# Kernel optimization log

Measured on AMD Instinct MI355X. Metric: run time of the kernel, lower is better.

The kernel has to match this reference:

```python
import jax, jax.numpy as jnp
import numpy as np

B = 32768
K = 8           # moe_num_experts
LATENT = 256    # latent_dim
COND = 1024     # fusion_hidden_dim
HID = 128       # moe_expert_hidden_dim
EIN = LATENT + COND + 1  # expert input dim = 1281


def setup_inputs() -> dict:
    key = jax.random.key(0)
    ks = jax.random.split(key, 12)
    cond = jax.random.normal(ks[0], (B, COND), dtype=jnp.float32)
    u = jax.random.normal(ks[1], (B, LATENT), dtype=jnp.float32)
    tau = jax.random.uniform(ks[2], (B, 1), dtype=jnp.float32)
    # posterior gate: positive, sums to 1 over K (realistic p_hat)
    p_raw = jax.random.uniform(ks[3], (B, K), dtype=jnp.float32)
    p_hat = p_raw / jnp.sum(p_raw, axis=-1, keepdims=True)
    s = 0.02
    W1 = jax.random.normal(ks[4], (K, EIN, HID), dtype=jnp.float32) * s
    b1 = jnp.zeros((K, HID), dtype=jnp.float32)
    W2 = jax.random.normal(ks[5], (K, HID, HID), dtype=jnp.float32) * s
    b2 = jnp.zeros((K, HID), dtype=jnp.float32)
    W3 = jax.random.normal(ks[6], (K, HID, LATENT), dtype=jnp.float32) * s
    b3 = jnp.zeros((K, LATENT), dtype=jnp.float32)
    return {"cond": cond, "u": u, "tau": tau, "p_hat": p_hat,
            "W1": W1, "b1": b1, "W2": W2, "b2": b2, "W3": W3, "b3": b3}


def reference(cond, u, tau, p_hat, W1, b1, W2, b2, W3, b3):
    # Training path: gate = p_hat (no smooth switching, no running gate).
    x = jnp.concatenate([u, cond, tau], axis=-1)           # (B, EIN)
    h = jax.nn.silu(jnp.einsum('bd,kdh->bkh', x, W1) + b1) # (B, K, HID)
    h = jax.nn.silu(jnp.einsum('bkh,khg->bkg', h, W2) + b2)
    v_experts = jnp.einsum('bkg,kgl->bkl', h, W3) + b3     # (B, K, LATENT)
    v = jnp.einsum('bk,bkl->bl', p_hat, v_experts)         # (B, LATENT)
    return v
```

## Files before the change

### kernel.cpp

```cpp
#include <hip/hip_runtime.h>
#include <stdint.h>

typedef unsigned short u16;
typedef __attribute__((ext_vector_type(8))) short short8;
typedef __attribute__((ext_vector_type(4))) float f32x4;
typedef __attribute__((ext_vector_type(4))) uint32_t u32x4;

#define KEXP   8
#define LATENT 256
#define CONDD  1024
#define HID    128
#define EIN    1281
#define EINP   1344
#define NCH    21
#define NTOT   1024
#define BROWS  32768

__device__ __forceinline__ u16 f2bf(float x) {
  uint32_t v = __float_as_uint(x);
  v += 0x7fffu + ((v >> 16) & 1u);
  return (u16)(v >> 16);
}

__device__ __forceinline__ void async16(const void* g, void* l) {
  __builtin_amdgcn_global_load_lds(
      (const __attribute__((address_space(1))) void*)g,
      (__attribute__((address_space(3))) void*)l, 16, 0, 0);
}

__device__ __forceinline__ float silu(float x) { return x / (1.f + __expf(-x)); }

#define W1_TILES (KEXP * 42 * 4)
#define W2_TILES (KEXP * 4 * 4)
#define W3_TILES (KEXP * 4 * 8)
#define WCONV_TILES (W1_TILES + W2_TILES + W3_TILES)
#define XGRP (BROWS * 168)
#define XBLK (XGRP / 256)

__global__ __launch_bounds__(256)
void prep(const float* __restrict__ W1, const float* __restrict__ W2,
          const float* __restrict__ W3, const float* __restrict__ cond,
          const float* __restrict__ uu, const float* __restrict__ tau,
          u16* __restrict__ W1t, u16* __restrict__ W2t, u16* __restrict__ W3t2,
          u16* __restrict__ Xbf) {
  __shared__ float t[32][33];
  const int bid = blockIdx.x;
  if (bid >= WCONV_TILES) {
    int g = (bid - WCONV_TILES) * 256 + threadIdx.x;
    int row = g / 168;
    int c8  = g - row * 168;
    float f0 = 0.f, f1 = 0.f, f2 = 0.f, f3 = 0.f, f4 = 0.f, f5 = 0.f, f6 = 0.f, f7 = 0.f;
    if (c8 < 32) {
      const float4* p = (const float4*)(uu + (size_t)row * LATENT + c8 * 8);
      float4 a = p[0], b = p[1];
      f0 = a.x; f1 = a.y; f2 = a.z; f3 = a.w; f4 = b.x; f5 = b.y; f6 = b.z; f7 = b.w;
    } else if (c8 < 160) {
      const float4* p = (const float4*)(cond + (size_t)row * CONDD + (c8 - 32) * 8);
      float4 a = p[0], b = p[1];
      f0 = a.x; f1 = a.y; f2 = a.z; f3 = a.w; f4 = b.x; f5 = b.y; f6 = b.z; f7 = b.w;
    } else if (c8 == 160) {
      f0 = tau[row];
    }
    u32x4 pk;
    pk[0] = (uint32_t)f2bf(f0) | ((uint32_t)f2bf(f1) << 16);
    pk[1] = (uint32_t)f2bf(f2) | ((uint32_t)f2bf(f3) << 16);
    pk[2] = (uint32_t)f2bf(f4) | ((uint32_t)f2bf(f5) << 16);
    pk[3] = (uint32_t)f2bf(f6) | ((uint32_t)f2bf(f7) << 16);
    *(u32x4*)(Xbf + (size_t)row * EINP + c8 * 8) = pk;
    return;
  }
  const int tx = threadIdx.x & 31, ty = threadIdx.x >> 5;
  if (bid < W1_TILES) {
    int k = bid / 168, r = bid % 168;
    int d0 = (r / 4) * 32, h0 = (r % 4) * 32;
    const float* src = W1 + (size_t)k * EIN * HID;
    #pragma unroll
    for (int s = 0; s < 4; ++s) {
      int d = d0 + ty + s * 8;
      t[ty + s * 8][tx] = (d < EIN) ? src[(size_t)d * HID + h0 + tx] : 0.f;
    }
    __syncthreads();
    u16* dst = W1t + (size_t)k * HID * EINP;
    #pragma unroll
    for (int s = 0; s < 4; ++s)
      dst[(size_t)(h0 + ty + s * 8) * EINP + d0 + tx] = f2bf(t[tx][ty + s * 8]);
  } else if (bid < W1_TILES + W2_TILES) {
    int j = bid - W1_TILES;
    int k = j / 16, r = j % 16;
    int d0 = (r / 4) * 32, h0 = (r % 4) * 32;
    const float* src = W2 + (size_t)k * HID * HID;
    #pragma unroll
    for (int s = 0; s < 4; ++s)
      t[ty + s * 8][tx] = src[(size_t)(d0 + ty + s * 8) * HID + h0 + tx];
    __syncthreads();
    u16* dst = W2t + (size_t)k * HID * HID;
    #pragma unroll
    for (int s = 0; s < 4; ++s)
      dst[(size_t)(h0 + ty + s * 8) * HID + d0 + tx] = f2bf(t[tx][ty + s * 8]);
  } else {
    int j = bid - W1_TILES - W2_TILES;
    int k = j / 32, r = j % 32;
    int d0 = (r / 8) * 32, h0 = (r % 8) * 32;
    const float* src = W3 + (size_t)k * HID * LATENT;
    #pragma unroll
    for (int s = 0; s < 4; ++s)
      t[ty + s * 8][tx] = src[(size_t)(d0 + ty + s * 8) * LATENT + h0 + tx];
    __syncthreads();
    #pragma unroll
    for (int s = 0; s < 4; ++s)
      W3t2[(size_t)(h0 + ty + s * 8) * NTOT + k * HID + d0 + tx] = f2bf(t[tx][ty + s * 8]);
  }
}

__global__ __launch_bounds__(256, 2)
void h1_fused(const u16* __restrict__ Xbf, const u16* __restrict__ W1t,
              const float* __restrict__ b1, const u16* __restrict__ W2t,
              const float* __restrict__ b2, const float* __restrict__ p_hat,
              u16* __restrict__ H) {
  __shared__ union {
    struct { u16 As[3][8192]; u16 Bs[2][8192]; } s;
    struct { u16 As2[16384]; u16 Bs2[2][8192]; } g;
    u16 Cs[128 * 72];
  } sm;

  const int tid  = threadIdx.x;
  const int wave = tid >> 6;
  const int lane = tid & 63;
  const int q    = lane >> 4;
  const int ln   = lane & 15;
  const int wm   = wave >> 1, wn = wave & 1;
  const int bid  = blockIdx.x;
  const int mt   = ((bid >> 6) << 3) | (bid & 7);
  const int e    = (bid >> 3) & 7;
  const int m0   = mt * 128;
  const u16* w1k = W1t + (size_t)e * HID * EINP;
  const u16* xtb = Xbf + (size_t)m0 * EINP;

  const f32x4 fz = {0.f, 0.f, 0.f, 0.f};
  f32x4 acc[4][4];
  #pragma unroll
  for (int m = 0; m < 4; ++m)
    #pragma unroll
    for (int n = 0; n < 4; ++n) acc[m][n] = fz;

  const int rloc = lane >> 3;
  const int gsw  = lane & 7;
  const int gsrc = gsw ^ rloc;

#define H1_SA(d0, buf) { \
  _Pragma("unroll") \
  for (int i_ = 0; i_ < 4; ++i_) { \
    int rb_ = (wave * 4 + i_) * 8; \
    async16(xtb + (size_t)(rb_ + rloc) * EINP + (d0) + gsrc * 8, &sm.s.As[buf][rb_ * 64]); \
  } }
#define H1_SB(d0, buf) { \
  _Pragma("unroll") \
  for (int i_ = 0; i_ < 4; ++i_) { \
    int rb_ = (wave * 4 + i_) * 8; \
    async16(w1k + (size_t)(rb_ + rloc) * EINP + (d0) + gsrc * 8, &sm.s.Bs[buf][rb_ * 64]); \
  } }

  auto mfma_chunk = [&](const u16* Ab, const u16* Bb) {
    __builtin_amdgcn_s_setprio(1);
    #pragma unroll
    for (int ks = 0; ks < 2; ++ks) {
      short8 a[4], b[4];
      #pragma unroll
      for (int m = 0; m < 4; ++m) {
        int r = wm * 64 + m * 16 + ln;
        int g = (ks * 4 + q) ^ (r & 7);
        a[m] = *(const short8*)(&Ab[r * 64 + g * 8]);
      }
      #pragma unroll
      for (int n = 0; n < 4; ++n) {
        int c = wn * 64 + n * 16 + ln;
        int g = (ks * 4 + q) ^ (c & 7);
        b[n] = *(const short8*)(&Bb[c * 64 + g * 8]);
      }
      #pragma unroll
      for (int m = 0; m < 4; ++m)
        #pragma unroll
        for (int n = 0; n < 4; ++n)
          acc[m][n] = __builtin_amdgcn_mfma_f32_16x16x32_bf16(a[m], b[n], acc[m][n], 0, 0, 0);
    }
    __builtin_amdgcn_s_setprio(0);
  };

#define H1_CH(trel, ac, bc, bp, ap, vm) \
  H1_SB(db + ((trel) + 1) * 64, bp); \
  H1_SA(db + ((trel) + 2) * 64, ap); \
  mfma_chunk(sm.s.As[ac], sm.s.Bs[bc]); \
  asm volatile("s_waitcnt vmcnt(" #vm ")" ::: "memory"); \
  __builtin_amdgcn_s_barrier(); \
  __builtin_amdgcn_sched_barrier(0);

  H1_SA(0, 0); H1_SB(0, 0); H1_SA(64, 1);
  asm volatile("s_waitcnt vmcnt(4)" ::: "memory");
  __builtin_amdgcn_s_barrier();
  __builtin_amdgcn_sched_barrier(0);

  #pragma unroll 1
  for (int j = 0; j < 3; ++j) {
    const int db = j * 384;
    H1_CH(0, 0, 0, 1, 2, 4)
    H1_CH(1, 1, 1, 0, 0, 4)
    H1_CH(2, 2, 0, 1, 1, 4)
    H1_CH(3, 0, 1, 0, 2, 4)
    H1_CH(4, 1, 0, 1, 0, 4)
    H1_CH(5, 2, 1, 0, 1, 4)
  }
  {
    const int db = 1152;
    H1_CH(0, 0, 0, 1, 2, 4)
    H1_SB(db + 128, 0);
    mfma_chunk(sm.s.As[1], sm.s.Bs[1]);
    asm volatile("s_waitcnt vmcnt(0)" ::: "memory");
    __builtin_amdgcn_s_barrier();
    __builtin_amdgcn_sched_barrier(0);
    mfma_chunk(sm.s.As[2], sm.s.Bs[0]);
  }
  __syncthreads();

  const u16* w2k = W2t + (size_t)e * HID * HID;
  #pragma unroll
  for (int kc = 0; kc < 2; ++kc)
    #pragma unroll
    for (int i = 0; i < 4; ++i) {
      int rbase = (wave * 4 + i) * 8;
      async16(w2k + (size_t)(rbase + rloc) * HID + kc * 64 + gsrc * 8,
              &sm.g.Bs2[kc][rbase * 64]);
    }

  float pr[4][4];
  #pragma unroll
  for (int m = 0; m < 4; ++m)
    #pragma unroll
    for (int r = 0; r < 4; ++r)
      pr[m][r] = p_hat[(size_t)(m0 + wm * 64 + m * 16 + q * 4 + r) * KEXP + e];

  #pragma unroll
  for (int n = 0; n < 4; ++n) {
    int cl = wn * 64 + n * 16 + ln;
    float bv = b1[e * HID + cl];
    #pragma unroll
    for (int m = 0; m < 4; ++m)
      #pragma unroll
      for (int r = 0; r < 4; ++r) {
        int row = wm * 64 + m * 16 + q * 4 + r;
        sm.g.As2[row * 128 + (((cl >> 3) ^ (row & 7)) << 3) + (cl & 7)] =
            f2bf(silu(acc[m][n][r] + bv));
      }
  }

  f32x4 acc2[4][4];
  #pragma unroll
  for (int m = 0; m < 4; ++m)
    #pragma unroll
    for (int n = 0; n < 4; ++n) acc2[m][n] = fz;

  __syncthreads();

  #pragma unroll
  for (int kc = 0; kc < 2; ++kc) {
    #pragma unroll
    for (int ks = 0; ks < 2; ++ks) {
      short8 a[4], b[4];
      #pragma unroll
      for (int m = 0; m < 4; ++m) {
        int r = wm * 64 + m * 16 + ln;
        int G = kc * 8 + ks * 4 + q;
        int g = (G & 8) | ((G ^ (r & 7)) & 7);
        a[m] = *(const short8*)(&sm.g.As2[r * 128 + g * 8]);
      }
      #pragma unroll
      for (int n = 0; n < 4; ++n) {
        int c = wn * 64 + n * 16 + ln;
        int g = (ks * 4 + q) ^ (c & 7);
        b[n] = *(const short8*)(&sm.g.Bs2[kc][c * 64 + g * 8]);
      }
      #pragma unroll
      for (int m = 0; m < 4; ++m)
        #pragma unroll
        for (int n = 0; n < 4; ++n)
          acc2[m][n] = __builtin_amdgcn_mfma_f32_16x16x32_bf16(a[m], b[n], acc2[m][n], 0, 0, 0);
    }
  }
  __syncthreads();

  u16* hb = H + (size_t)m0 * NTOT + e * HID;
  #pragma unroll 1
  for (int hf = 0; hf < 2; ++hf) {
    if (wn == hf) {
      #pragma unroll
      for (int n = 0; n < 4; ++n) {
        int cl = n * 16 + ln;
        float bv = b2[e * HID + hf * 64 + cl];
        #pragma unroll
        for (int m = 0; m < 4; ++m)
          #pragma unroll
          for (int r = 0; r < 4; ++r) {
            int row = wm * 64 + m * 16 + q * 4 + r;
            sm.Cs[row * 72 + cl] = f2bf(pr[m][r] * silu(acc2[m][n][r] + bv));
          }
      }
    }
    __syncthreads();
    #pragma unroll
    for (int i = 0; i < 4; ++i) {
      int lin = tid + i * 256;
      int row = lin >> 3;
      int grp = lin & 7;
      *(u32x4*)(hb + (size_t)row * NTOT + hf * 64 + grp * 8) =
          *(const u32x4*)(&sm.Cs[row * 72 + grp * 8]);
    }
    __syncthreads();
  }
#undef H1_SA
#undef H1_SB
#undef H1_CH
}

__global__ __launch_bounds__(256, 2)
void out_gemm(const u16* __restrict__ H, const float* __restrict__ p_hat,
              const u16* __restrict__ W3t2, const float* __restrict__ b3,
              float* __restrict__ out) {
  __shared__ struct {
    u16 As[3][4096];
    u16 Bs[3][8192];
    float Ps[64 * 8];
    float B3s[128 * 8];
  } sm;

  const int tid  = threadIdx.x;
  const int wave = tid >> 6;
  const int lane = tid & 63;
  const int q    = lane >> 4;
  const int ln   = lane & 15;
  const int bid  = blockIdx.x;
  const int mt   = ((bid >> 4) << 3) | (bid & 7);
  const int bn   = (bid >> 3) & 1;
  const int m0   = mt * 64, n0 = bn * 128;

  if (tid < 128) {
    int row = tid >> 1, h = tid & 1;
    *(float4*)(&sm.Ps[row * 8 + h * 4]) = *(const float4*)(p_hat + (size_t)(m0 + row) * KEXP + h * 4);
  }
  #pragma unroll
  for (int i = 0; i < 4; ++i) {
    int k = i * 2 + (tid >> 7);
    int c = tid & 127;
    sm.B3s[c * 8 + k] = b3[k * LATENT + n0 + c];
  }

  const f32x4 fz = {0.f, 0.f, 0.f, 0.f};
  f32x4 acc[4][2];
  #pragma unroll
  for (int m = 0; m < 4; ++m) { acc[m][0] = fz; acc[m][1] = fz; }

  const int rloc = lane >> 3;
  const int gsw  = lane & 7;
  const int gsrc = gsw ^ rloc;

#define OG_SA(d0, buf) { \
  _Pragma("unroll") \
  for (int i_ = 0; i_ < 2; ++i_) { \
    int rb_ = (wave * 2 + i_) * 8; \
    async16(H + (size_t)(m0 + rb_ + rloc) * NTOT + (d0) + gsrc * 8, &sm.As[buf][rb_ * 64]); \
  } }
#define OG_SB(d0, buf) { \
  _Pragma("unroll") \
  for (int i_ = 0; i_ < 4; ++i_) { \
    int rb_ = (wave * 4 + i_) * 8; \
    async16(W3t2 + (size_t)(n0 + rb_ + rloc) * NTOT + (d0) + gsrc * 8, &sm.Bs[buf][rb_ * 64]); \
  } }

  auto mfma_chunk = [&](const u16* Ab, const u16* Bb) {
    __builtin_amdgcn_s_setprio(1);
    #pragma unroll
    for (int ks = 0; ks < 2; ++ks) {
      short8 a[4], b[2];
      #pragma unroll
      for (int m = 0; m < 4; ++m) {
        int r = m * 16 + ln;
        int g = (ks * 4 + q) ^ (r & 7);
        a[m] = *(const short8*)(&Ab[r * 64 + g * 8]);
      }
      #pragma unroll
      for (int n = 0; n < 2; ++n) {
        int c = wave * 32 + n * 16 + ln;
        int g = (ks * 4 + q) ^ (c & 7);
        b[n] = *(const short8*)(&Bb[c * 64 + g * 8]);
      }
      #pragma unroll
      for (int m = 0; m < 4; ++m)
        #pragma unroll
        for (int n = 0; n < 2; ++n)
          acc[m][n] = __builtin_amdgcn_mfma_f32_16x16x32_bf16(a[m], b[n], acc[m][n], 0, 0, 0);
    }
    __builtin_amdgcn_s_setprio(0);
  };

#define OG_CH(trel, ac, ap) \
  OG_SB(db + ((trel) + 2) * 64, ap); \
  OG_SA(db + ((trel) + 2) * 64, ap); \
  mfma_chunk(sm.As[ac], sm.Bs[ac]); \
  asm volatile("s_waitcnt vmcnt(6)" ::: "memory"); \
  __builtin_amdgcn_s_barrier(); \
  __builtin_amdgcn_sched_barrier(0);

  OG_SA(0, 0); OG_SB(0, 0);
  OG_SA(64, 1); OG_SB(64, 1);
  asm volatile("s_waitcnt vmcnt(6)" ::: "memory");
  __builtin_amdgcn_s_barrier();
  __builtin_amdgcn_sched_barrier(0);

  #pragma unroll 1
  for (int j = 0; j < 4; ++j) {
    const int db = j * 192;
    OG_CH(0, 0, 2)
    OG_CH(1, 1, 0)
    OG_CH(2, 2, 1)
  }
  {
    const int db = 768;
    OG_CH(0, 0, 2)
    OG_CH(1, 1, 0)
    mfma_chunk(sm.As[2], sm.Bs[2]);
    asm volatile("s_waitcnt vmcnt(0)" ::: "memory");
    __builtin_amdgcn_s_barrier();
    __builtin_amdgcn_sched_barrier(0);
    mfma_chunk(sm.As[0], sm.Bs[0]);
  }

  #pragma unroll
  for (int n = 0; n < 2; ++n) {
    int col = wave * 32 + n * 16 + ln;
    float4 c0 = *(const float4*)(&sm.B3s[col * 8]);
    float4 c1 = *(const float4*)(&sm.B3s[col * 8 + 4]);
    #pragma unroll
    for (int m = 0; m < 4; ++m)
      #pragma unroll
      for (int r = 0; r < 4; ++r) {
        int row = m * 16 + q * 4 + r;
        float4 p0 = *(const float4*)(&sm.Ps[row * 8]);
        float4 p1 = *(const float4*)(&sm.Ps[row * 8 + 4]);
        float v = acc[m][n][r]
                + p0.x * c0.x + p0.y * c0.y + p0.z * c0.z + p0.w * c0.w
                + p1.x * c1.x + p1.y * c1.y + p1.z * c1.z + p1.w * c1.w;
        out[(size_t)(m0 + row) * LATENT + n0 + col] = v;
      }
  }
#undef OG_SA
#undef OG_SB
#undef OG_CH
}

__global__ __launch_bounds__(256, 4)
void h1_gemm(const float* __restrict__ cond, const float* __restrict__ uu,
             const float* __restrict__ tau, const u16* __restrict__ W1t,
             const float* __restrict__ b1, u16* __restrict__ H1) {
  __shared__ union {
    struct { u16 As[128 * 64]; u16 Bs[128 * 64]; } s;
    u16 Cs[128 * 72];
  } sm;

  const int tid  = threadIdx.x;
  const int wave = tid >> 6;
  const int lane = tid & 63;
  const int q    = lane >> 4;
  const int ln   = lane & 15;
  const int wm   = wave >> 1, wn = wave & 1;
  const int bid  = blockIdx.x;
  const int mt   = ((bid >> 6) << 3) | (bid & 7);
  const int e    = (bid >> 3) & 7;
  const int m0   = mt * 128, n0 = e * 128;
  const u16* w1k = W1t + (size_t)e * HID * EINP;

  const f32x4 fz = {0.f, 0.f, 0.f, 0.f};
  f32x4 acc[4][4];
  #pragma unroll
  for (int m = 0; m < 4; ++m)
    #pragma unroll
    for (int n = 0; n < 4; ++n) acc[m][n] = fz;

  #pragma unroll 1
  for (int ic = 0; ic < NCH; ++ic) {
    const int d0 = ic * 64;
    #pragma unroll
    for (int i = 0; i < 4; ++i) {
      int lin  = tid + i * 256;
      int row  = lin >> 3;
      int gsw  = lin & 7;
      int gsrc = gsw ^ (row & 7);
      int gr   = m0 + row;
      float f0, f1, f2, f3, f4, f5, f6, f7;
      if (d0 < 256) {
        const float4* p = (const float4*)(uu + (size_t)gr * LATENT + d0 + gsrc * 8);
        float4 A = p[0], Bv = p[1];
        f0 = A.x; f1 = A.y; f2 = A.z; f3 = A.w; f4 = Bv.x; f5 = Bv.y; f6 = Bv.z; f7 = Bv.w;
      } else if (d0 < 1280) {
        const float4* p = (const float4*)(cond + (size_t)gr * CONDD + (d0 - 256) + gsrc * 8);
        float4 A = p[0], Bv = p[1];
        f0 = A.x; f1 = A.y; f2 = A.z; f3 = A.w; f4 = Bv.x; f5 = Bv.y; f6 = Bv.z; f7 = Bv.w;
      } else {
        float tv = tau[gr];
        f0 = (gsrc == 0) ? tv : 0.f;
        f1 = f2 = f3 = f4 = f5 = f6 = f7 = 0.f;
      }
      u32x4 pk;
      pk[0] = (uint32_t)f2bf(f0) | ((uint32_t)f2bf(f1) << 16);
      pk[1] = (uint32_t)f2bf(f2) | ((uint32_t)f2bf(f3) << 16);
      pk[2] = (uint32_t)f2bf(f4) | ((uint32_t)f2bf(f5) << 16);
      pk[3] = (uint32_t)f2bf(f6) | ((uint32_t)f2bf(f7) << 16);
      *(u32x4*)(&sm.s.As[row * 64 + gsw * 8]) = pk;
    }
    {
      int rloc = lane >> 3;
      int gsw  = lane & 7;
      int gsrc = gsw ^ rloc;
      #pragma unroll
      for (int i = 0; i < 4; ++i) {
        int rbase = (wave * 4 + i) * 8;
        async16(w1k + (size_t)(rbase + rloc) * EINP + d0 + gsrc * 8,
                &sm.s.Bs[rbase * 64]);
      }
    }
    __syncthreads();
    #pragma unroll
    for (int ks = 0; ks < 2; ++ks) {
      short8 a[4], b[4];
      #pragma unroll
      for (int m = 0; m < 4; ++m) {
        int r = wm * 64 + m * 16 + ln;
        int g = (ks * 4 + q) ^ (r & 7);
        a[m] = *(const short8*)(&sm.s.As[r * 64 + g * 8]);
      }
      #pragma unroll
      for (int n = 0; n < 4; ++n) {
        int c = wn * 64 + n * 16 + ln;
        int g = (ks * 4 + q) ^ (c & 7);
        b[n] = *(const short8*)(&sm.s.Bs[c * 64 + g * 8]);
      }
      #pragma unroll
      for (int m = 0; m < 4; ++m)
        #pragma unroll
        for (int n = 0; n < 4; ++n)
          acc[m][n] = __builtin_amdgcn_mfma_f32_16x16x32_bf16(a[m], b[n], acc[m][n], 0, 0, 0);
    }
    __syncthreads();
  }

  #pragma unroll 1
  for (int hf = 0; hf < 2; ++hf) {
    if (wn == hf) {
      #pragma unroll
      for (int n = 0; n < 4; ++n) {
        int cl = n * 16 + ln;
        float bv = b1[n0 + hf * 64 + cl];
        #pragma unroll
        for (int m = 0; m < 4; ++m)
          #pragma unroll
          for (int r = 0; r < 4; ++r)
            sm.Cs[(wm * 64 + m * 16 + q * 4 + r) * 72 + cl] = f2bf(silu(acc[m][n][r] + bv));
      }
    }
    __syncthreads();
    #pragma unroll
    for (int i = 0; i < 4; ++i) {
      int lin = tid + i * 256;
      int row = lin >> 3;
      int grp = lin & 7;
      *(u32x4*)(H1 + (size_t)(m0 + row) * NTOT + n0 + hf * 64 + grp * 8) =
          *(const u32x4*)(&sm.Cs[row * 72 + grp * 8]);
    }
    __syncthreads();
  }
}

__global__ __launch_bounds__(256, 4)
void h2_gemm(u16* __restrict__ H, const float* __restrict__ p_hat,
             const u16* __restrict__ W2t, const float* __restrict__ b2) {
  __shared__ struct {
    union { struct { u16 As[128 * 64]; u16 Bs[128 * 64]; } s; u16 Cs[128 * 72]; } u;
    float Ps[128];
  } sm;

  const int tid  = threadIdx.x;
  const int wave = tid >> 6;
  const int lane = tid & 63;
  const int q    = lane >> 4;
  const int ln   = lane & 15;
  const int wm   = wave >> 1, wn = wave & 1;
  const int mt   = blockIdx.x >> 3;
  const int e    = blockIdx.x & 7;
  const int row0 = mt * 128;

  if (tid < 128) sm.Ps[tid] = p_hat[(size_t)(row0 + tid) * KEXP + e];

  const u16* w2k = W2t + (size_t)e * HID * HID;
  u16* hb = H + (size_t)row0 * NTOT + e * HID;

  const f32x4 fz = {0.f, 0.f, 0.f, 0.f};
  f32x4 acc[4][4];
  #pragma unroll
  for (int m = 0; m < 4; ++m)
    #pragma unroll
    for (int n = 0; n < 4; ++n) acc[m][n] = fz;

  const int rloc = lane >> 3;
  const int gsw  = lane & 7;
  const int gsrc = gsw ^ rloc;

  #pragma unroll 1
  for (int kc = 0; kc < 2; ++kc) {
    #pragma unroll
    for (int i = 0; i < 4; ++i) {
      int rbase = (wave * 4 + i) * 8;
      async16(hb + (size_t)(rbase + rloc) * NTOT + kc * 64 + gsrc * 8,
              &sm.u.s.As[rbase * 64]);
      async16(w2k + (size_t)(rbase + rloc) * HID + kc * 64 + gsrc * 8,
              &sm.u.s.Bs[rbase * 64]);
    }
    __syncthreads();
    #pragma unroll
    for (int ks = 0; ks < 2; ++ks) {
      short8 a[4], b[4];
      #pragma unroll
      for (int m = 0; m < 4; ++m) {
        int r = wm * 64 + m * 16 + ln;
        int g = (ks * 4 + q) ^ (r & 7);
        a[m] = *(const short8*)(&sm.u.s.As[r * 64 + g * 8]);
      }
      #pragma unroll
      for (int n = 0; n < 4; ++n) {
        int c = wn * 64 + n * 16 + ln;
        int g = (ks * 4 + q) ^ (c & 7);
        b[n] = *(const short8*)(&sm.u.s.Bs[c * 64 + g * 8]);
      }
      #pragma unroll
      for (int m = 0; m < 4; ++m)
        #pragma unroll
        for (int n = 0; n < 4; ++n)
          acc[m][n] = __builtin_amdgcn_mfma_f32_16x16x32_bf16(a[m], b[n], acc[m][n], 0, 0, 0);
    }
    __syncthreads();
  }

  #pragma unroll 1
  for (int hf = 0; hf < 2; ++hf) {
    if (wn == hf) {
      #pragma unroll
      for (int n = 0; n < 4; ++n) {
        int cl = n * 16 + ln;
        float bv = b2[e * HID + hf * 64 + cl];
        #pragma unroll
        for (int m = 0; m < 4; ++m)
          #pragma unroll
          for (int r = 0; r < 4; ++r) {
            int row = wm * 64 + m * 16 + q * 4 + r;
            sm.u.Cs[row * 72 + cl] = f2bf(sm.Ps[row] * silu(acc[m][n][r] + bv));
          }
      }
    }
    __syncthreads();
    #pragma unroll
    for (int i = 0; i < 4; ++i) {
      int lin = tid + i * 256;
      int row = lin >> 3;
      int grp = lin & 7;
      *(u32x4*)(hb + (size_t)row * NTOT + hf * 64 + grp * 8) =
          *(const u32x4*)(&sm.u.Cs[row * 72 + grp * 8]);
    }
    __syncthreads();
  }
}

extern "C" void kernel_launch(void* const* d_in, const int* in_sizes, int n_in,
                              void* d_out, int out_size, void* d_ws, size_t ws_size,
                              hipStream_t stream) {
  const float* cond  = (const float*)d_in[0];
  const float* u     = (const float*)d_in[1];
  const float* tau   = (const float*)d_in[2];
  const float* p_hat = (const float*)d_in[3];
  const float* W1    = (const float*)d_in[4];
  const float* b1    = (const float*)d_in[5];
  const float* W2    = (const float*)d_in[6];
  const float* b2    = (const float*)d_in[7];
  const float* W3    = (const float*)d_in[8];
  const float* b3    = (const float*)d_in[9];
  float* out = (float*)d_out;

  const size_t N1 = (size_t)KEXP * HID * EINP;
  const size_t N2 = (size_t)KEXP * HID * HID;
  const size_t N3 = (size_t)LATENT * NTOT;
  const size_t NH = (size_t)BROWS * NTOT;
  const size_t NX = (size_t)BROWS * EINP;

  u16* W1t  = (u16*)d_ws;
  u16* W2t  = W1t + N1;
  u16* W3t2 = W2t + N2;
  u16* H    = W3t2 + N3;

  if (ws_size >= (N1 + N2 + N3 + NH + NX) * sizeof(u16)) {
    u16* Xbf = H + NH;
    prep<<<WCONV_TILES + XBLK, 256, 0, stream>>>(W1, W2, W3, cond, u, tau,
                                                 W1t, W2t, W3t2, Xbf);
    h1_fused<<<2048, 256, 0, stream>>>(Xbf, W1t, b1, W2t, b2, p_hat, H);
    out_gemm<<<1024, 256, 0, stream>>>(H, p_hat, W3t2, b3, out);
  } else if (ws_size >= (N1 + N2 + N3 + NH) * sizeof(u16)) {
    prep<<<WCONV_TILES, 256, 0, stream>>>(W1, W2, W3, cond, u, tau,
                                          W1t, W2t, W3t2, (u16*)nullptr);
    h1_gemm<<<2048, 256, 0, stream>>>(cond, u, tau, W1t, b1, H);
    h2_gemm<<<2048, 256, 0, stream>>>(H, p_hat, W2t, b2);
    out_gemm<<<1024, 256, 0, stream>>>(H, p_hat, W3t2, b3, out);
  }
}
```

Baseline: 403.7 us.

## Enlarge out_gemm tile to 128x128 with 2x2 wave grid and split A/B buffering

The final GEMM (H times W3 into the latent output) now uses 128x128 block tiles instead of 64x128, with waves arranged 2x2 and each wave computing a 64x64 sub-tile. The grid halves to 512 blocks. Buffering changes to triple-buffered A and double-buffered B, with B prefetched one chunk ahead. The bias/p_hat epilogue now reads b3 and p_hat straight from global into registers instead of staging them in LDS. The aim is more MFMA work per LDS load and less global traffic for H and W3, at the cost of more accumulator registers and fewer blocks, which may lower occupancy.

```diff
diff --git a/kernel.cpp b/kernel.cpp
--- a/kernel.cpp
+++ b/kernel.cpp
@@ -325,10 +325,8 @@
               const u16* __restrict__ W3t2, const float* __restrict__ b3,
               float* __restrict__ out) {
   __shared__ struct {
-    u16 As[3][4096];
-    u16 Bs[3][8192];
-    float Ps[64 * 8];
-    float B3s[128 * 8];
+    u16 As[3][8192];
+    u16 Bs[2][8192];
   } sm;
 
   const int tid  = threadIdx.x;
@@ -336,26 +334,20 @@
   const int lane = tid & 63;
   const int q    = lane >> 4;
   const int ln   = lane & 15;
+  const int wm   = wave >> 1, wn = wave & 1;
   const int bid  = blockIdx.x;
   const int mt   = ((bid >> 4) << 3) | (bid & 7);
   const int bn   = (bid >> 3) & 1;
-  const int m0   = mt * 64, n0 = bn * 128;
-
-  if (tid < 128) {
-    int row = tid >> 1, h = tid & 1;
-    *(float4*)(&sm.Ps[row * 8 + h * 4]) = *(const float4*)(p_hat + (size_t)(m0 + row) * KEXP + h * 4);
-  }
-  #pragma unroll
-  for (int i = 0; i < 4; ++i) {
-    int k = i * 2 + (tid >> 7);
-    int c = tid & 127;
-    sm.B3s[c * 8 + k] = b3[k * LATENT + n0 + c];
-  }
+  const int m0   = mt * 128, n0 = bn * 128;
+  const u16* hb  = H + (size_t)m0 * NTOT;
+  const u16* w3b = W3t2 + (size_t)n0 * NTOT;
 
   const f32x4 fz = {0.f, 0.f, 0.f, 0.f};
-  f32x4 acc[4][2];
-  #pragma unroll
-  for (int m = 0; m < 4; ++m) { acc[m][0] = fz; acc[m][1] = fz; }
+  f32x4 acc[4][4];
+  #pragma unroll
+  for (int m = 0; m < 4; ++m)
+    #pragma unroll
+    for (int n = 0; n < 4; ++n) acc[m][n] = fz;
 
   const int rloc = lane >> 3;
   const int gsw  = lane & 7;
@@ -363,93 +355,101 @@
 
 #define OG_SA(d0, buf) { \
   _Pragma("unroll") \
-  for (int i_ = 0; i_ < 2; ++i_) { \
-    int rb_ = (wave * 2 + i_) * 8; \
-    async16(H + (size_t)(m0 + rb_ + rloc) * NTOT + (d0) + gsrc * 8, &sm.As[buf][rb_ * 64]); \
+  for (int i_ = 0; i_ < 4; ++i_) { \
+    int rb_ = (wave * 4 + i_) * 8; \
+    async16(hb + (size_t)(rb_ + rloc) * NTOT + (d0) + gsrc * 8, &sm.As[buf][rb_ * 64]); \
   } }
 #define OG_SB(d0, buf) { \
   _Pragma("unroll") \
   for (int i_ = 0; i_ < 4; ++i_) { \
     int rb_ = (wave * 4 + i_) * 8; \
-    async16(W3t2 + (size_t)(n0 + rb_ + rloc) * NTOT + (d0) + gsrc * 8, &sm.Bs[buf][rb_ * 64]); \
+    async16(w3b + (size_t)(rb_ + rloc) * NTOT + (d0) + gsrc * 8, &sm.Bs[buf][rb_ * 64]); \
   } }
 
   auto mfma_chunk = [&](const u16* Ab, const u16* Bb) {
     __builtin_amdgcn_s_setprio(1);
     #pragma unroll
     for (int ks = 0; ks < 2; ++ks) {
-      short8 a[4], b[2];
+      short8 a[4], b[4];
       #pragma unroll
       for (int m = 0; m < 4; ++m) {
-        int r = m * 16 + ln;
+        int r = wm * 64 + m * 16 + ln;
         int g = (ks * 4 + q) ^ (r & 7);
         a[m] = *(const short8*)(&Ab[r * 64 + g * 8]);
       }
       #pragma unroll
-      for (int n = 0; n < 2; ++n) {
-        int c = wave * 32 + n * 16 + ln;
+      for (int n = 0; n < 4; ++n) {
+        int c = wn * 64 + n * 16 + ln;
         int g = (ks * 4 + q) ^ (c & 7);
         b[n] = *(const short8*)(&Bb[c * 64 + g * 8]);
       }
       #pragma unroll
       for (int m = 0; m < 4; ++m)
         #pragma unroll
-        for (int n = 0; n < 2; ++n)
+        for (int n = 0; n < 4; ++n)
           acc[m][n] = __builtin_amdgcn_mfma_f32_16x16x32_bf16(a[m], b[n], acc[m][n], 0, 0, 0);
     }
     __builtin_amdgcn_s_setprio(0);
   };
 
-#define OG_CH(trel, ac, ap) \
-  OG_SB(db + ((trel) + 2) * 64, ap); \
+#define OG_CH(trel, ac, bc, bp, ap, vm) \
+  OG_SB(db + ((trel) + 1) * 64, bp); \
   OG_SA(db + ((trel) + 2) * 64, ap); \
-  mfma_chunk(sm.As[ac], sm.Bs[ac]); \
-  asm volatile("s_waitcnt vmcnt(6)" ::: "memory"); \
+  mfma_chunk(sm.As[ac], sm.Bs[bc]); \
+  asm volatile("s_waitcnt vmcnt(" #vm ")" ::: "memory"); \
   __builtin_amdgcn_s_barrier(); \
   __builtin_amdgcn_sched_barrier(0);
 
-  OG_SA(0, 0); OG_SB(0, 0);
-  OG_SA(64, 1); OG_SB(64, 1);
-  asm volatile("s_waitcnt vmcnt(6)" ::: "memory");
+  OG_SA(0, 0); OG_SB(0, 0); OG_SA(64, 1);
+  asm volatile("s_waitcnt vmcnt(4)" ::: "memory");
   __builtin_amdgcn_s_barrier();
   __builtin_amdgcn_sched_barrier(0);
 
   #pragma unroll 1
-  for (int j = 0; j < 4; ++j) {
-    const int db = j * 192;
-    OG_CH(0, 0, 2)
-    OG_CH(1, 1, 0)
-    OG_CH(2, 2, 1)
+  for (int j = 0; j < 2; ++j) {
+    const int db = j * 384;
+    OG_CH(0, 0, 0, 1, 2, 4)
+    OG_CH(1, 1, 1, 0, 0, 4)
+    OG_CH(2, 2, 0, 1, 1, 4)
+    OG_CH(3, 0, 1, 0, 2, 4)
+    OG_CH(4, 1, 0, 1, 0, 4)
+    OG_CH(5, 2, 1, 0, 1, 4)
   }
   {
     const int db = 768;
-    OG_CH(0, 0, 2)
-    OG_CH(1, 1, 0)
-    mfma_chunk(sm.As[2], sm.Bs[2]);
+    OG_CH(0, 0, 0, 1, 2, 4)
+    OG_CH(1, 1, 1, 0, 0, 4)
+    OG_SB(db + 192, 1);
+    mfma_chunk(sm.As[2], sm.Bs[0]);
     asm volatile("s_waitcnt vmcnt(0)" ::: "memory");
     __builtin_amdgcn_s_barrier();
     __builtin_amdgcn_sched_barrier(0);
-    mfma_chunk(sm.As[0], sm.Bs[0]);
-  }
-
-  #pragma unroll
-  for (int n = 0; n < 2; ++n) {
-    int col = wave * 32 + n * 16 + ln;
-    float4 c0 = *(const float4*)(&sm.B3s[col * 8]);
-    float4 c1 = *(const float4*)(&sm.B3s[col * 8 + 4]);
-    #pragma unroll
-    for (int m = 0; m < 4; ++m)
-      #pragma unroll
-      for (int r = 0; r < 4; ++r) {
-        int row = m * 16 + q * 4 + r;
-        float4 p0 = *(const float4*)(&sm.Ps[row * 8]);
-        float4 p1 = *(const float4*)(&sm.Ps[row * 8 + 4]);
+    mfma_chunk(sm.As[0], sm.Bs[1]);
+  }
+
+  float b3c[4][8];
+  #pragma unroll
+  for (int n = 0; n < 4; ++n) {
+    int gcol = n0 + wn * 64 + n * 16 + ln;
+    #pragma unroll
+    for (int k = 0; k < 8; ++k) b3c[n][k] = b3[k * LATENT + gcol];
+  }
+  #pragma unroll
+  for (int m = 0; m < 4; ++m)
+    #pragma unroll
+    for (int r = 0; r < 4; ++r) {
+      int grow = m0 + wm * 64 + m * 16 + q * 4 + r;
+      float4 p0 = *(const float4*)(p_hat + (size_t)grow * KEXP);
+      float4 p1 = *(const float4*)(p_hat + (size_t)grow * KEXP + 4);
+      #pragma unroll
+      for (int n = 0; n < 4; ++n) {
+        int gcol = n0 + wn * 64 + n * 16 + ln;
         float v = acc[m][n][r]
-                + p0.x * c0.x + p0.y * c0.y + p0.z * c0.z + p0.w * c0.w
-                + p1.x * c1.x + p1.y * c1.y + p1.z * c1.z + p1.w * c1.w;
-        out[(size_t)(m0 + row) * LATENT + n0 + col] = v;
-      }
-  }
+                + p0.x * b3c[n][0] + p0.y * b3c[n][1] + p0.z * b3c[n][2] + p0.w * b3c[n][3]
+                + p1.x * b3c[n][4] + p1.y * b3c[n][5] + p1.z * b3c[n][6] + p1.w * b3c[n][7];
+        out[(size_t)grow * LATENT + gcol] = v;
+      }
+    }
 #undef OG_SA
 #undef OG_SB
 #undef OG_CH
@@ -706,12 +706,12 @@
     prep<<<WCONV_TILES + XBLK, 256, 0, stream>>>(W1, W2, W3, cond, u, tau,
                                                  W1t, W2t, W3t2, Xbf);
     h1_fused<<<2048, 256, 0, stream>>>(Xbf, W1t, b1, W2t, b2, p_hat, H);
-    out_gemm<<<1024, 256, 0, stream>>>(H, p_hat, W3t2, b3, out);
+    out_gemm<<<512, 256, 0, stream>>>(H, p_hat, W3t2, b3, out);
   } else if (ws_size >= (N1 + N2 + N3 + NH) * sizeof(u16)) {
     prep<<<WCONV_TILES, 256, 0, stream>>>(W1, W2, W3, cond, u, tau,
                                           W1t, W2t, W3t2, (u16*)nullptr);
     h1_gemm<<<2048, 256, 0, stream>>>(cond, u, tau, W1t, b1, H);
     h2_gemm<<<2048, 256, 0, stream>>>(H, p_hat, W2t, b2);
-    out_gemm<<<1024, 256, 0, stream>>>(H, p_hat, W3t2, b3, out);
+    out_gemm<<<512, 256, 0, stream>>>(H, p_hat, W3t2, b3, out);
   }
 }
```

Measured after the change: 395.2 us. 1.02x faster.
